# Optimization experiments

Measured on AMD Instinct MI355X. Metric: run time of the kernel, lower is better.

The kernel has to match this reference:

```python
import jax, jax.numpy as jnp
import numpy as np

B, S, D = 1, 2048, 4096          # batch, seqlen, model dim
H, KVH, HD = 32, 8, 128          # query heads, kv heads, head dim
W = 1024                         # sliding window
ROPE_THETA = 10000.0


def _rope(t, cos, sin):
    # t: [b, s, h, hd]; complex pairing matches torch.view_as_complex on reshape(..., hd//2, 2)
    a = t[..., 0::2]
    b = t[..., 1::2]
    out_r = a * cos - b * sin
    out_i = a * sin + b * cos
    return jnp.stack([out_r, out_i], axis=-1).reshape(t.shape)


def setup_inputs() -> dict:
    key = jax.random.key(0)
    ks = jax.random.split(key, 5)
    x = jax.random.normal(ks[0], (1, B, S, D), dtype=jnp.float32)
    wq = jax.random.normal(ks[1], (H * HD, D), dtype=jnp.float32) * 0.02
    wk = jax.random.normal(ks[2], (KVH * HD, D), dtype=jnp.float32) * 0.02
    wv = jax.random.normal(ks[3], (KVH * HD, D), dtype=jnp.float32) * 0.02
    wo = jax.random.normal(ks[4], (D, H * HD), dtype=jnp.float32) * 0.02
    # rotary frequencies: freqs_cis[s, hd/2] = exp(i * s * theta^{-2k/hd})
    inv_freq = 1.0 / (ROPE_THETA ** (jnp.arange(0, HD, 2, dtype=jnp.float32) / HD))
    angles = jnp.arange(S, dtype=jnp.float32)[:, None] * inv_freq[None, :]  # [S, HD/2]
    freqs_cos = jnp.cos(angles)
    freqs_sin = jnp.sin(angles)
    # sliding-window causal mask (additive)
    i = jnp.arange(S)
    allowed = (i[:, None] >= i[None, :]) & (i[:, None] - i[None, :] < W)
    mask = jnp.where(allowed, 0.0, -1e9).astype(jnp.float32)
    positions = jnp.arange(S, dtype=jnp.int64)
    return {"x": x, "wq": wq, "wk": wk, "wv": wv, "wo": wo,
            "freqs_cos": freqs_cos, "freqs_sin": freqs_sin,
            "mask": mask, "positions": positions}


def reference(x, wq, wk, wv, wo, freqs_cos, freqs_sin, mask, positions):
    xs = x[0]                                   # [B, S, D]
    xq = (xs @ wq.T).reshape(B, S, H, HD)
    xk = (xs @ wk.T).reshape(B, S, KVH, HD)
    xv = (xs @ wv.T).reshape(B, S, KVH, HD)
    cos = freqs_cos[None, :, None, :]           # [1, S, 1, HD/2]
    sin = freqs_sin[None, :, None, :]
    xq = _rope(xq, cos, sin)
    xk = _rope(xk, cos, sin)
    # GQA: repeat_interleave kv heads to match query heads (prefill path)
    rep = H // KVH
    k = jnp.repeat(xk, rep, axis=2)             # [B, S, H, HD]
    v = jnp.repeat(xv, rep, axis=2)
    scale = HD ** -0.5
    scores = jnp.einsum('bqhd,bkhd->bhqk', xq, k) * scale + mask[None, None]
    probs = jax.nn.softmax(scores, axis=-1)
    out = jnp.einsum('bhqk,bkhd->bqhd', probs, v).reshape(B, S, H * HD)
    return (out @ wo.T)[None]                   # [1, B, S, D]
```

## Files before the change

kernel.cpp:

```cpp
#include <hip/hip_runtime.h>
#include <hip/hip_bf16.h>


typedef __attribute__((ext_vector_type(8))) short short8;
typedef __attribute__((ext_vector_type(4))) float floatx4;
typedef unsigned short u16;
typedef unsigned int u32;

__device__ __forceinline__ u16 f2bf(float f) {
  u32 u = __builtin_bit_cast(u32, f);
  u32 r = u + 0x7FFFu + ((u >> 16) & 1u);
  return (u16)(r >> 16);
}

#define GLDS16(g, l)                                                     \
  __builtin_amdgcn_global_load_lds(                                      \
      (const __attribute__((address_space(1))) u32*)(g),                 \
      (__attribute__((address_space(3))) u32*)(l), 16, 0, 0)

__global__ __launch_bounds__(256) void cast_all(
    const float* __restrict__ x, const float* __restrict__ wq,
    const float* __restrict__ wk, const float* __restrict__ wv,
    const float* __restrict__ wo, u16* __restrict__ xb, u16* __restrict__ wqb,
    u16* __restrict__ wkb, u16* __restrict__ wvb, u16* __restrict__ wob) {
  const int tid = blockIdx.x * blockDim.x + threadIdx.x;
  const int stride = gridDim.x * blockDim.x;
  auto seg = [&](const float* __restrict__ in, u16* __restrict__ out, int n4) {
    for (int i = tid; i < n4; i += stride) {
      float4 v = ((const float4*)in)[i];
      ushort4 o;
      o.x = f2bf(v.x); o.y = f2bf(v.y); o.z = f2bf(v.z); o.w = f2bf(v.w);
      ((ushort4*)out)[i] = o;
    }
  };
  seg(x, xb, 2097152);
  seg(wq, wqb, 4194304);
  seg(wk, wkb, 1048576);
  seg(wv, wvb, 1048576);
  seg(wo, wob, 4194304);
}

template <int IS_QKV>
__global__ __launch_bounds__(512, 2) void gemm_t(
    const u16* __restrict__ A, const u16* __restrict__ B, void* __restrict__ Cq,
    u16* __restrict__ Ck, u16* __restrict__ Cv, const float* __restrict__ fcos,
    const float* __restrict__ fsin) {
  constexpr int BN = IS_QKV ? 192 : 128;
  constexpr int NFR = BN / 64;
  constexpr int WC = BN / 4;
  constexpr int BUFSZ = 16384 + BN * 64;
  __shared__ u16 lds[3 * BUFSZ / 2];
  const int K = 4096;

  const int bm = blockIdx.x & 7;
  const int bx = blockIdx.x >> 3;
  const int m0 = bm * 256, n0 = bx * BN;

  const int t = threadIdx.x, l = t & 63, w = t >> 6;
  const int li = l & 15, g = l >> 4;
  const int wm = w >> 2, wn = w & 3;

  const int rr = t >> 2;
  const int ssw = (t & 3) ^ ((rr >> 1) & 3);
  const u16* gA = A + (size_t)(m0 + rr) * K + ssw * 8;
  const u16* gB = B + (size_t)(n0 + rr) * K + ssw * 8;
  const int dA = t * 16;

  auto stage = [&](int p, int kt) {
    char* base = (char*)lds + p * BUFSZ;
    GLDS16(gA + kt, base + dA);
    GLDS16(gA + (size_t)128 * K + kt, base + 8192 + dA);
    GLDS16(gB + kt, base + 16384 + dA);
    if constexpr (IS_QKV) {
      if (t < 256)
        GLDS16(gB + (size_t)128 * K + kt, base + 24576 + dA);
    }
  };
  auto waitL = [&]() {
    if constexpr (IS_QKV) {
      if (t < 256) asm volatile("s_waitcnt vmcnt(4)" ::: "memory");
      else         asm volatile("s_waitcnt vmcnt(3)" ::: "memory");
    } else {
      asm volatile("s_waitcnt vmcnt(3)" ::: "memory");
    }
  };

  int offA[8], offB[NFR];
#pragma unroll
  for (int mf = 0; mf < 8; mf++) {
    int r = wm * 128 + mf * 16 + li;
    offA[mf] = r * 64 + ((g ^ ((r >> 1) & 3)) << 4);
  }
#pragma unroll
  for (int nf = 0; nf < NFR; nf++) {
    int r = wn * WC + nf * 16 + li;
    offB[nf] = 16384 + r * 64 + ((g ^ ((r >> 1) & 3)) << 4);
  }

  floatx4 acc[8][NFR] = {};
  const int NT = K / 32;

  stage(0, 0);
  stage(1, 32);
  waitL();
  __builtin_amdgcn_s_barrier();

  int p = 0;
  for (int tt = 0; tt < NT; ++tt) {
    int p2 = p + 2; if (p2 >= 3) p2 -= 3;
    const char* ab = (const char*)lds + p * BUFSZ;
    short8 afr[8], bfr[NFR];
#pragma unroll
    for (int mf = 0; mf < 8; mf++) afr[mf] = *(const short8*)(ab + offA[mf]);
#pragma unroll
    for (int nf = 0; nf < NFR; nf++) bfr[nf] = *(const short8*)(ab + offB[nf]);
    if (tt + 2 < NT) stage(p2, (tt + 2) * 32);
    __builtin_amdgcn_sched_barrier(0);
    __builtin_amdgcn_s_barrier();
    asm volatile("s_waitcnt lgkmcnt(0)" ::: "memory");
    __builtin_amdgcn_sched_barrier(0);
    __builtin_amdgcn_s_setprio(1);
#pragma unroll
    for (int mf = 0; mf < 8; mf++)
#pragma unroll
      for (int nf = 0; nf < NFR; nf++)
        acc[mf][nf] = __builtin_amdgcn_mfma_f32_16x16x32_bf16(afr[mf], bfr[nf], acc[mf][nf], 0, 0, 0);
    __builtin_amdgcn_s_setprio(0);
    if (tt + 2 < NT) {
      waitL();
    } else if (tt + 1 < NT) {
      asm volatile("s_waitcnt vmcnt(0)" ::: "memory");
    }
    __builtin_amdgcn_sched_barrier(0);
    __builtin_amdgcn_s_barrier();
    p = p + 1; if (p >= 3) p -= 3;
  }

  const float scale = 0.08838834764831845f;
#pragma unroll
  for (int mf = 0; mf < 8; mf++) {
#pragma unroll
    for (int nf = 0; nf < NFR; nf++) {
      const int row0 = m0 + wm * 128 + mf * 16 + 4 * g;
      const int c = n0 + wn * WC + nf * 16 + li;
      if constexpr (!IS_QKV) {
        float* Cf = (float*)Cq;
#pragma unroll
        for (int r = 0; r < 4; r++) Cf[(size_t)(row0 + r) * 4096 + c] = acc[mf][nf][r];
      } else {
        if (c < 5120) {
          const int hd = c & 127;
          const int pp = hd >> 1;
          const bool even = (hd & 1) == 0;
#pragma unroll
          for (int r = 0; r < 4; r++) {
            const int row = row0 + r;
            float cv = fcos[row * 64 + pp];
            float sv = fsin[row * 64 + pp];
            float v = acc[mf][nf][r];
            float pv = __shfl_xor(v, 1);
            float o = even ? (v * cv - pv * sv) : (pv * sv + v * cv);
            if (c < 4096) {
              ((u16*)Cq)[(size_t)row * 4096 + c] = f2bf(o * scale);
            } else {
              Ck[(size_t)row * 1024 + (c - 4096)] = f2bf(o);
            }
          }
        } else {
          u32 lo = (u32)f2bf(acc[mf][nf][0]) | ((u32)f2bf(acc[mf][nf][1]) << 16);
          u32 hi = (u32)f2bf(acc[mf][nf][2]) | ((u32)f2bf(acc[mf][nf][3]) << 16);
          uint2 val; val.x = lo; val.y = hi;
          *(uint2*)(&Cv[(size_t)(c - 5120) * 2048 + row0]) = val;
        }
      }
    }
  }
}

__global__ __launch_bounds__(256) void attn_kernel(const u16* __restrict__ Q,
                                                   const u16* __restrict__ K,
                                                   const u16* __restrict__ Vt,
                                                   u16* __restrict__ O) {
  __shared__ u16 Ks[2][64 * 128];
  __shared__ u16 Vs[2][128 * 64];
  __shared__ u16 Ps[4][16 * 72];

  const int t = threadIdx.x, l = t & 63, w = t >> 6;
  const int li = l & 15, g = l >> 4;
  const int q0 = blockIdx.x * 64;
  const int h = blockIdx.y;
  const int kvh = h >> 2;
  const int qw = q0 + w * 16;

  short8 qf[4];
  {
    const u16* qp = Q + (size_t)(qw + li) * 4096 + h * 128 + g * 8;
#pragma unroll
    for (int kk = 0; kk < 4; kk++) qf[kk] = *(const short8*)(qp + kk * 32);
  }

  const u16* gK[4];
  const u16* gV[4];
  int ldsOff[4];
#pragma unroll
  for (int i = 0; i < 4; i++) {
    int rK = 16 * w + 4 * i + (l >> 4);
    int sK = (l & 15) ^ (rK & 7);
    gK[i] = K + (size_t)rK * 1024 + kvh * 128 + sK * 8;
    int rV = 32 * w + 8 * i + (l >> 3);
    int sV = (l & 7) ^ (rV & 7);
    gV[i] = Vt + (size_t)(kvh * 128 + rV) * 2048 + sV * 8;
    ldsOff[i] = (4 * w + i) * 1024;
  }

  int offK[4][4];
#pragma unroll
  for (int n = 0; n < 4; n++) {
    int r = 16 * n + li;
#pragma unroll
    for (int kk = 0; kk < 4; kk++)
      offK[n][kk] = r * 256 + (((kk * 4 + g) ^ (r & 7)) << 4);
  }
  int offV[2][8];
#pragma unroll
  for (int kb = 0; kb < 2; kb++)
#pragma unroll
    for (int dt = 0; dt < 8; dt++) {
      int d = dt * 16 + li;
      offV[kb][dt] = d * 128 + (((kb * 4 + g) ^ (d & 7)) << 4);
    }

  float mrow[4] = {-1e30f, -1e30f, -1e30f, -1e30f};
  float lsum[4] = {0.f, 0.f, 0.f, 0.f};
  floatx4 accO[8] = {};

  int klo = q0 - 1023;
  if (klo < 0) klo = 0;
  klo &= ~63;
  const int nt = (q0 + 64 - klo) >> 6;

  auto stage = [&](int buf, int k0) {
    char* ksb = (char*)&Ks[buf][0];
    char* vsb = (char*)&Vs[buf][0];
#pragma unroll
    for (int i = 0; i < 4; i++) GLDS16(gK[i] + (size_t)k0 * 1024, ksb + ldsOff[i]);
#pragma unroll
    for (int i = 0; i < 4; i++) GLDS16(gV[i] + k0, vsb + ldsOff[i]);
  };

  stage(0, klo);
  asm volatile("s_waitcnt vmcnt(0)" ::: "memory");
  __builtin_amdgcn_s_barrier();

  for (int it = 0; it < nt; it++) {
    const int k0 = klo + (it << 6);
    if (it + 1 < nt) stage((it + 1) & 1, k0 + 64);

    if (k0 <= qw + 15 && k0 + 63 >= qw - 1023) {
      const char* kb = (const char*)&Ks[it & 1][0];
      const char* vb = (const char*)&Vs[it & 1][0];
      floatx4 s[4] = {};
      __builtin_amdgcn_s_setprio(1);
#pragma unroll
      for (int kk = 0; kk < 4; kk++)
#pragma unroll
        for (int n = 0; n < 4; n++) {
          short8 kf = *(const short8*)(kb + offK[n][kk]);
          s[n] = __builtin_amdgcn_mfma_f32_16x16x32_bf16(qf[kk], kf, s[n], 0, 0, 0);
        }
      __builtin_amdgcn_s_setprio(0);
      const bool full = (k0 + 63 <= qw) && (k0 >= qw + 15 - 1023);
      if (!full) {
#pragma unroll
        for (int n = 0; n < 4; n++) {
          const int kc = k0 + n * 16 + li;
#pragma unroll
          for (int r = 0; r < 4; r++) {
            const int qr = qw + 4 * g + r;
            if (kc > qr || qr - kc > 1023) s[n][r] = -__builtin_inff();
          }
        }
      }
      float rm[4];
#pragma unroll
      for (int r = 0; r < 4; r++)
        rm[r] = fmaxf(fmaxf(s[0][r], s[1][r]), fmaxf(s[2][r], s[3][r]));
#pragma unroll
      for (int msk = 1; msk <= 8; msk <<= 1)
#pragma unroll
        for (int r = 0; r < 4; r++) rm[r] = fmaxf(rm[r], __shfl_xor(rm[r], msk));
      float al[4];
#pragma unroll
      for (int r = 0; r < 4; r++) {
        float mn = fmaxf(mrow[r], rm[r]);
        al[r] = __expf(mrow[r] - mn);
        mrow[r] = mn;
        lsum[r] *= al[r];
      }
#pragma unroll
      for (int dt = 0; dt < 8; dt++)
#pragma unroll
        for (int r = 0; r < 4; r++) accO[dt][r] *= al[r];
      float rs[4] = {0.f, 0.f, 0.f, 0.f};
      u16* pw = &Ps[w][0];
#pragma unroll
      for (int n = 0; n < 4; n++)
#pragma unroll
        for (int r = 0; r < 4; r++) {
          float p = __expf(s[n][r] - mrow[r]);
          rs[r] += p;
          pw[(4 * g + r) * 72 + n * 16 + li] = f2bf(p);
        }
#pragma unroll
      for (int msk = 1; msk <= 8; msk <<= 1)
#pragma unroll
        for (int r = 0; r < 4; r++) rs[r] += __shfl_xor(rs[r], msk);
#pragma unroll
      for (int r = 0; r < 4; r++) lsum[r] += rs[r];
      short8 pa[2];
#pragma unroll
      for (int kbi = 0; kbi < 2; kbi++)
        pa[kbi] = *(const short8*)((const char*)&Ps[w][0] + li * 144 + kbi * 64 + g * 16);
      __builtin_amdgcn_s_setprio(1);
#pragma unroll
      for (int kbi = 0; kbi < 2; kbi++)
#pragma unroll
        for (int dt = 0; dt < 8; dt++) {
          short8 vf = *(const short8*)(vb + offV[kbi][dt]);
          accO[dt] = __builtin_amdgcn_mfma_f32_16x16x32_bf16(pa[kbi], vf, accO[dt], 0, 0, 0);
        }
      __builtin_amdgcn_s_setprio(0);
    }
    asm volatile("s_waitcnt vmcnt(0)" ::: "memory");
    __builtin_amdgcn_s_barrier();
  }

  float inv[4];
#pragma unroll
  for (int r = 0; r < 4; r++) inv[r] = 1.0f / lsum[r];
#pragma unroll
  for (int dt = 0; dt < 8; dt++)
#pragma unroll
    for (int r = 0; r < 4; r++)
      O[(size_t)(qw + 4 * g + r) * 4096 + h * 128 + dt * 16 + li] =
          f2bf(accO[dt][r] * inv[r]);
}

extern "C" void kernel_launch(void* const* d_in, const int* in_sizes, int n_in,
                              void* d_out, int out_size, void* d_ws, size_t ws_size,
                              hipStream_t stream) {
  const float* x    = (const float*)d_in[0];
  const float* wq   = (const float*)d_in[1];
  const float* wk   = (const float*)d_in[2];
  const float* wv   = (const float*)d_in[3];
  const float* wo   = (const float*)d_in[4];
  const float* fcos = (const float*)d_in[5];
  const float* fsin = (const float*)d_in[6];

  u16* ws  = (u16*)d_ws;
  u16* xb  = ws;
  u16* wqb = xb + 8388608;
  u16* wkb = wqb + 16777216;
  u16* wvb = wkb + 4194304;
  u16* wob = wvb + 4194304;
  u16* Qb  = wob + 16777216;
  u16* Kb  = Qb + 8388608;
  u16* Vtb = Kb + 2097152;
  u16* AOb = Vtb + 2097152;

  cast_all<<<2048, 256, 0, stream>>>(x, wq, wk, wv, wo, xb, wqb, wkb, wvb, wob);
  gemm_t<1><<<256, 512, 0, stream>>>(xb, wqb, Qb, Kb, Vtb, fcos, fsin);
  attn_kernel<<<dim3(32, 32), 256, 0, stream>>>(Qb, Kb, Vtb, AOb);
  gemm_t<0><<<256, 512, 0, stream>>>(AOb, wob, d_out, nullptr, nullptr, nullptr, nullptr);
}
```

Measured before the change: 336.8 us.

## Split GEMM main loop into two half-phases interleaving LDS reads, prefetch and MFMA

Each K-step of the bf16 GEMM main loop is split into two phases. The first loads B fragments plus half of the A fragments, issues the A prefetch and runs half the MFMAs. The second loads the remaining A fragments, issues the B prefetch and runs the other half. This aims to cut register pressure for A fragments and to interleave global-to-LDS traffic with compute more finely. It adds an extra pair of barriers per iteration and keeps the same vmcnt wait logic.

```diff
diff --git a/kernel.cpp b/kernel.cpp
--- a/kernel.cpp
+++ b/kernel.cpp
@@ -66,10 +66,13 @@
   const u16* gB = B + (size_t)(n0 + rr) * K + ssw * 8;
   const int dA = t * 16;
 
-  auto stage = [&](int p, int kt) {
+  auto stageA = [&](int p, int kt) {
     char* base = (char*)lds + p * BUFSZ;
     GLDS16(gA + kt, base + dA);
     GLDS16(gA + (size_t)128 * K + kt, base + 8192 + dA);
+  };
+  auto stageB = [&](int p, int kt) {
+    char* base = (char*)lds + p * BUFSZ;
     GLDS16(gB + kt, base + 16384 + dA);
     if constexpr (IS_QKV) {
       if (t < 256)
@@ -100,8 +103,8 @@
   floatx4 acc[8][NFR] = {};
   const int NT = K / 32;
 
-  stage(0, 0);
-  stage(1, 32);
+  stageA(0, 0); stageB(0, 0);
+  stageA(1, 32); stageB(1, 32);
   waitL();
   __builtin_amdgcn_s_barrier();
 
@@ -109,24 +112,42 @@
   for (int tt = 0; tt < NT; ++tt) {
     int p2 = p + 2; if (p2 >= 3) p2 -= 3;
     const char* ab = (const char*)lds + p * BUFSZ;
-    short8 afr[8], bfr[NFR];
-#pragma unroll
-    for (int mf = 0; mf < 8; mf++) afr[mf] = *(const short8*)(ab + offA[mf]);
+    const int kt2 = (tt + 2) * 32;
+    const bool pre = (tt + 2 < NT);
+    short8 afr[4], bfr[NFR];
 #pragma unroll
     for (int nf = 0; nf < NFR; nf++) bfr[nf] = *(const short8*)(ab + offB[nf]);
-    if (tt + 2 < NT) stage(p2, (tt + 2) * 32);
+#pragma unroll
+    for (int mf = 0; mf < 4; mf++) afr[mf] = *(const short8*)(ab + offA[mf]);
+    if (pre) stageA(p2, kt2);
     __builtin_amdgcn_sched_barrier(0);
     __builtin_amdgcn_s_barrier();
     asm volatile("s_waitcnt lgkmcnt(0)" ::: "memory");
     __builtin_amdgcn_sched_barrier(0);
     __builtin_amdgcn_s_setprio(1);
 #pragma unroll
-    for (int mf = 0; mf < 8; mf++)
+    for (int mf = 0; mf < 4; mf++)
 #pragma unroll
       for (int nf = 0; nf < NFR; nf++)
         acc[mf][nf] = __builtin_amdgcn_mfma_f32_16x16x32_bf16(afr[mf], bfr[nf], acc[mf][nf], 0, 0, 0);
     __builtin_amdgcn_s_setprio(0);
-    if (tt + 2 < NT) {
+    __builtin_amdgcn_sched_barrier(0);
+    __builtin_amdgcn_s_barrier();
+#pragma unroll
+    for (int mf = 0; mf < 4; mf++) afr[mf] = *(const short8*)(ab + offA[4 + mf]);
+    if (pre) stageB(p2, kt2);
+    __builtin_amdgcn_sched_barrier(0);
+    __builtin_amdgcn_s_barrier();
+    asm volatile("s_waitcnt lgkmcnt(0)" ::: "memory");
+    __builtin_amdgcn_sched_barrier(0);
+    __builtin_amdgcn_s_setprio(1);
+#pragma unroll
+    for (int mf = 0; mf < 4; mf++)
+#pragma unroll
+      for (int nf = 0; nf < NFR; nf++)
+        acc[4 + mf][nf] = __builtin_amdgcn_mfma_f32_16x16x32_bf16(afr[mf], bfr[nf], acc[4 + mf][nf], 0, 0, 0);
+    __builtin_amdgcn_s_setprio(0);
+    if (pre) {
       waitL();
     } else if (tt + 1 < NT) {
       asm volatile("s_waitcnt vmcnt(0)" ::: "memory");
```

After: 338.4 us. About the same (+0.5%).
